# Performance work log

Hardware: AMD Instinct MI355X
Metric: run time of the kernel (lower is better)

## Reference

```python
import jax, jax.numpy as jnp
import numpy as np

N_EMBED = 384
HEAD_SIZE = 64
B, T = 128, 512


def rope(x):
    # Faithful to source: fres = 1/1000**(arange(0,dim,2)//dim) -> integer
    # floor-div makes the exponent all zeros, so fres == 1 everywhere.
    Bx, Tx, D = x.shape
    half = D // 2
    fres = jnp.ones((half,), dtype=jnp.float32)
    ang = jnp.arange(Tx, dtype=jnp.float32)[:, None] * fres[None, :]  # (T, half)
    cos, sin = jnp.cos(ang), jnp.sin(ang)
    xr = x.reshape(Bx, Tx, half, 2)
    xe, xo = xr[..., 0], xr[..., 1]
    oe = xe * cos - xo * sin
    oo = xe * sin + xo * cos
    return jnp.stack([oe, oo], axis=-1).reshape(Bx, Tx, D)


def setup_inputs() -> dict:
    key = jax.random.key(0)
    ks = jax.random.split(key, 7)
    s = 1.0 / np.sqrt(N_EMBED)
    return {
        "x": jax.random.normal(ks[0], (B, T, N_EMBED), dtype=jnp.float32),
        "wq": jax.random.uniform(ks[1], (N_EMBED, HEAD_SIZE), jnp.float32, -s, s),
        "bq": jax.random.uniform(ks[2], (HEAD_SIZE,), jnp.float32, -s, s),
        "wk": jax.random.uniform(ks[3], (N_EMBED, HEAD_SIZE), jnp.float32, -s, s),
        "bk": jax.random.uniform(ks[4], (HEAD_SIZE,), jnp.float32, -s, s),
        "wv": jax.random.uniform(ks[5], (N_EMBED, HEAD_SIZE), jnp.float32, -s, s),
        "bv": jax.random.uniform(ks[6], (HEAD_SIZE,), jnp.float32, -s, s),
    }


def reference(x, wq, bq, wk, bk, wv, bv):
    Bx, Tx, C = x.shape  # C = n_embed; scale uses C per the source (not head_size)
    q = rope(x @ wq + bq)
    k = rope(x @ wk + bk)
    wei = jnp.einsum("bqd,bkd->bqk", q, k) * (C ** -0.5)  # (B, T, T)
    causal = jnp.tril(jnp.ones((Tx, Tx), dtype=bool))
    wei = jnp.where(causal, wei, -jnp.inf)
    wei = jax.nn.softmax(wei, axis=-1)
    v = x @ wv + bv
    return jnp.einsum("bqk,bkd->bqd", wei, v)
```

## Files before the change

kernel.cpp:

```cpp
#include <hip/hip_runtime.h>

#define TSEQ 512
#define NB   128
#define CDIM 384
#define HD   64
#define QSCALE 0.051031036307982884f
#define MBIAS  8.0f

typedef _Float16 half8  __attribute__((ext_vector_type(8)));
typedef _Float16 half4  __attribute__((ext_vector_type(4)));
typedef float    floatx4 __attribute__((ext_vector_type(4)));

typedef __attribute__((address_space(3))) unsigned int lds_u32;
typedef const __attribute__((address_space(1))) unsigned int g_u32;

__device__ __forceinline__ void load_lds16(const void* g, void* l) {
    __builtin_amdgcn_global_load_lds((g_u32*)g, (lds_u32*)l, 16, 0, 0);
}

__global__ void prep_w(const float* __restrict__ wq, const float* __restrict__ wk,
                       const float* __restrict__ wv, _Float16* __restrict__ Wt)
{
    int i = blockIdx.x * 256 + threadIdx.x;
    const int per = CDIM * HD;
    if (i >= 3 * per) return;
    int mat = i / per;
    int rem = i - mat * per;
    int k = rem / HD;
    int n = rem - k * HD;
    const float* w = (mat == 0) ? wq : ((mat == 1) ? wk : wv);
    Wt[((size_t)mat * HD + n) * CDIM + k] = (_Float16)w[rem];
}

__global__ __launch_bounds__(256) void qkv_gemm(
    const float* __restrict__ x, const _Float16* __restrict__ Wt,
    const float* __restrict__ bq, const float* __restrict__ bk,
    const float* __restrict__ bv,
    _Float16* __restrict__ Qw, _Float16* __restrict__ Kw,
    _Float16* __restrict__ Vtw, int b0)
{
    __shared__ __align__(16) float    xs[8 * 64 * 8];
    __shared__ __align__(16) _Float16 wsb[8 * 192 * 8];

    const int tid  = threadIdx.x;
    const int wave = tid >> 6;
    const int lane = tid & 63;
    const int l16  = lane & 15;
    const int quad = lane >> 4;

    const int row0 = blockIdx.x * 64;
    const size_t rowg = (size_t)b0 * TSEQ + row0;

    floatx4 acc[12];
#pragma unroll
    for (int i = 0; i < 12; ++i)
#pragma unroll
        for (int r = 0; r < 4; ++r) acc[i][r] = 0.f;

    for (int c = 0; c < 6; ++c) {
        const int kk0 = c * 64;

#pragma unroll
        for (int i = 0; i < 4; ++i) {
            const int I    = wave * 4 + i;
            const int cell = I * 32 + (lane >> 1);
            const int kblk = cell >> 6;
            const int m    = cell & 63;
            const int kin0 = (lane & 1) * 4;
            const float* src = x + (rowg + m) * CDIM + kk0 + kblk * 8 + kin0;
            load_lds16(src, (char*)xs + I * 1024);
        }
#pragma unroll
        for (int i = 0; i < 6; ++i) {
            const int I2   = wave * 6 + i;
            const int c2   = I2 * 64 + lane;
            const int kblk = c2 / 192;
            const int n    = c2 - kblk * 192;
            const _Float16* src = Wt + (size_t)n * CDIM + kk0 + kblk * 8;
            load_lds16(src, (char*)wsb + I2 * 1024);
        }
        __syncthreads();

#pragma unroll
        for (int kb2 = 0; kb2 < 2; ++kb2) {
            const int kblk = kb2 * 4 + quad;
            const float* ap = xs + ((size_t)kblk * 64 + wave * 16 + l16) * 8;
            floatx4 a0 = *(const floatx4*)ap;
            floatx4 a1 = *(const floatx4*)(ap + 4);
            half8 a;
#pragma unroll
            for (int jj = 0; jj < 8; ++jj)
                a[jj] = (_Float16)(jj < 4 ? a0[jj] : a1[jj - 4]);
            const _Float16* bp = wsb + ((size_t)kblk * 192 + l16) * 8;
#pragma unroll
            for (int i = 0; i < 12; ++i) {
                half8 bb = *(const half8*)(bp + i * 128);
                acc[i] = __builtin_amdgcn_mfma_f32_16x16x32_f16(a, bb, acc[i], 0, 0, 0);
            }
        }
        __syncthreads();
    }

    float bq4[4], bk4[4], bv4[4];
#pragma unroll
    for (int s4 = 0; s4 < 4; ++s4) {
        const int cc = s4 * 16 + l16;
        bq4[s4] = bq[cc]; bk4[s4] = bk[cc]; bv4[s4] = bv[cc];
    }
    const int t00  = (row0 & (TSEQ - 1)) + wave * 16 + quad * 4;
    const int bidx = row0 >> 9;
    const int rowb = row0 + wave * 16 + quad * 4;

#pragma unroll
    for (int r = 0; r < 4; ++r) {
        const int t = t00 + r;
        const float st = sinf((float)t);
        const float ct = cosf((float)t);
        const int row = rowb + r;
#pragma unroll
        for (int s4 = 0; s4 < 4; ++s4) {
            const int cc = s4 * 16 + l16;
            float vq = acc[s4][r] + bq4[s4];
            float pq = __shfl_xor(vq, 1);
            vq = (cc & 1) ? (pq * st + vq * ct) : (vq * ct - pq * st);
            Qw[(size_t)row * HD + cc] = (_Float16)(vq * QSCALE);
            float vk = acc[4 + s4][r] + bk4[s4];
            float pk = __shfl_xor(vk, 1);
            vk = (cc & 1) ? (pk * st + vk * ct) : (vk * ct - pk * st);
            Kw[(size_t)row * HD + cc] = (_Float16)vk;
        }
    }
#pragma unroll
    for (int s4 = 0; s4 < 4; ++s4) {
        const int cc = s4 * 16 + l16;
        half4 vpack;
#pragma unroll
        for (int r = 0; r < 4; ++r) vpack[r] = (_Float16)(acc[8 + s4][r] + bv4[s4]);
        *(half4*)(Vtw + ((size_t)bidx * HD + cc) * TSEQ + t00) = vpack;
    }
}

__global__ __launch_bounds__(256) void attn_kernel(
    const _Float16* __restrict__ Qw, const _Float16* __restrict__ Kw,
    const _Float16* __restrict__ Vtw, float* __restrict__ out, int b0)
{
    const int qt   = blockIdx.x;
    const int bl   = blockIdx.y;
    const int tid  = threadIdx.x;
    const int wave = tid >> 6;
    const int lane = tid & 63;
    const int l16  = lane & 15;
    const int quad = lane >> 4;

    __shared__ __align__(16) _Float16 pbuf[4][16][72];

    const _Float16* Qb = Qw  + (size_t)bl * TSEQ * HD;
    const _Float16* Kb = Kw  + (size_t)bl * TSEQ * HD;
    const _Float16* Vb = Vtw + (size_t)bl * HD * TSEQ;

    const int qA = qt * 128 + wave * 16;
    const int qB = qA + 64;
    const int jd = 2 * qt;

    half8 aQA0 = *(const half8*)(Qb + (size_t)(qA + l16) * HD + quad * 8);
    half8 aQA1 = *(const half8*)(Qb + (size_t)(qA + l16) * HD + 32 + quad * 8);
    half8 aQB0 = *(const half8*)(Qb + (size_t)(qB + l16) * HD + quad * 8);
    half8 aQB1 = *(const half8*)(Qb + (size_t)(qB + l16) * HD + 32 + quad * 8);

    half8 ones;
#pragma unroll
    for (int jj = 0; jj < 8; ++jj) ones[jj] = (_Float16)1.f;

    floatx4 accO[8], accL[2];
#pragma unroll
    for (int i = 0; i < 8; ++i)
#pragma unroll
        for (int r = 0; r < 4; ++r) accO[i][r] = 0.f;
#pragma unroll
    for (int s = 0; s < 2; ++s)
#pragma unroll
        for (int r = 0; r < 4; ++r) accL[s][r] = 0.f;

    for (int j = 0; j <= jd + 1; ++j) {
        const int kb = j * 64;

        half8 bK0[4], bK1[4], bV0[4], bV1[4];
#pragma unroll
        for (int s4 = 0; s4 < 4; ++s4) {
            const _Float16* kp = Kb + (size_t)(kb + s4 * 16 + l16) * HD + quad * 8;
            bK0[s4] = *(const half8*)(kp);
            bK1[s4] = *(const half8*)(kp + 32);
            const _Float16* vp = Vb + (size_t)(s4 * 16 + l16) * TSEQ + kb + quad * 8;
            bV0[s4] = *(const half8*)(vp);
            bV1[s4] = *(const half8*)(vp + 32);
        }

        if (j <= jd) {
            floatx4 st4[4];
#pragma unroll
            for (int s4 = 0; s4 < 4; ++s4) {
#pragma unroll
                for (int r = 0; r < 4; ++r) st4[s4][r] = 0.f;
                st4[s4] = __builtin_amdgcn_mfma_f32_16x16x32_f16(bK0[s4], aQA0, st4[s4], 0, 0, 0);
                st4[s4] = __builtin_amdgcn_mfma_f32_16x16x32_f16(bK1[s4], aQA1, st4[s4], 0, 0, 0);
            }
            const int qrow = qA + l16;
#pragma unroll
            for (int s4 = 0; s4 < 4; ++s4) {
                half4 w;
#pragma unroll
                for (int r = 0; r < 4; ++r) {
                    float p = __expf(fminf(st4[s4][r], 18.f) - MBIAS);
                    if (j == jd) {
                        const int kcol = kb + s4 * 16 + quad * 4 + r;
                        if (kcol > qrow) p = 0.f;
                    }
                    w[r] = (_Float16)p;
                }
                *(half4*)(&pbuf[wave][l16][s4 * 16 + quad * 4]) = w;
            }
            half8 aP0 = *(const half8*)(&pbuf[wave][l16][quad * 8]);
            half8 aP1 = *(const half8*)(&pbuf[wave][l16][32 + quad * 8]);
#pragma unroll
            for (int s4 = 0; s4 < 4; ++s4) {
                accO[s4] = __builtin_amdgcn_mfma_f32_16x16x32_f16(aP0, bV0[s4], accO[s4], 0, 0, 0);
                accO[s4] = __builtin_amdgcn_mfma_f32_16x16x32_f16(aP1, bV1[s4], accO[s4], 0, 0, 0);
            }
            accL[0] = __builtin_amdgcn_mfma_f32_16x16x32_f16(aP0, ones, accL[0], 0, 0, 0);
            accL[0] = __builtin_amdgcn_mfma_f32_16x16x32_f16(aP1, ones, accL[0], 0, 0, 0);
        }

        {
            floatx4 st4[4];
#pragma unroll
            for (int s4 = 0; s4 < 4; ++s4) {
#pragma unroll
                for (int r = 0; r < 4; ++r) st4[s4][r] = 0.f;
                st4[s4] = __builtin_amdgcn_mfma_f32_16x16x32_f16(bK0[s4], aQB0, st4[s4], 0, 0, 0);
                st4[s4] = __builtin_amdgcn_mfma_f32_16x16x32_f16(bK1[s4], aQB1, st4[s4], 0, 0, 0);
            }
            const int qrow = qB + l16;
#pragma unroll
            for (int s4 = 0; s4 < 4; ++s4) {
                half4 w;
#pragma unroll
                for (int r = 0; r < 4; ++r) {
                    float p = __expf(fminf(st4[s4][r], 18.f) - MBIAS);
                    if (j == jd + 1) {
                        const int kcol = kb + s4 * 16 + quad * 4 + r;
                        if (kcol > qrow) p = 0.f;
                    }
                    w[r] = (_Float16)p;
                }
                *(half4*)(&pbuf[wave][l16][s4 * 16 + quad * 4]) = w;
            }
            half8 aP0 = *(const half8*)(&pbuf[wave][l16][quad * 8]);
            half8 aP1 = *(const half8*)(&pbuf[wave][l16][32 + quad * 8]);
#pragma unroll
            for (int s4 = 0; s4 < 4; ++s4) {
                accO[4 + s4] = __builtin_amdgcn_mfma_f32_16x16x32_f16(aP0, bV0[s4], accO[4 + s4], 0, 0, 0);
                accO[4 + s4] = __builtin_amdgcn_mfma_f32_16x16x32_f16(aP1, bV1[s4], accO[4 + s4], 0, 0, 0);
            }
            accL[1] = __builtin_amdgcn_mfma_f32_16x16x32_f16(aP0, ones, accL[1], 0, 0, 0);
            accL[1] = __builtin_amdgcn_mfma_f32_16x16x32_f16(aP1, ones, accL[1], 0, 0, 0);
        }
    }

#pragma unroll
    for (int s = 0; s < 2; ++s) {
        const int qbase = (s == 0) ? qA : qB;
        float inv[4];
#pragma unroll
        for (int r = 0; r < 4; ++r) inv[r] = 1.f / accL[s][r];
#pragma unroll
        for (int s4 = 0; s4 < 4; ++s4) {
            const int dcol = s4 * 16 + l16;
#pragma unroll
            for (int r = 0; r < 4; ++r) {
                const int qr = qbase + quad * 4 + r;
                out[((size_t)(b0 + bl) * TSEQ + qr) * HD + dcol] =
                    accO[s * 4 + s4][r] * inv[r];
            }
        }
    }
}

extern "C" void kernel_launch(void* const* d_in, const int* in_sizes, int n_in,
                              void* d_out, int out_size, void* d_ws, size_t ws_size,
                              hipStream_t stream)
{
    char* ws = (char*)d_ws;
    _Float16* Wt = (_Float16*)ws;
    char* qkv_base = ws + 147456;

    const size_t per_b = (size_t)3 * TSEQ * HD * sizeof(_Float16);
    size_t avail = (ws_size > (size_t)147456) ? ws_size - 147456 : per_b;
    int nbc = (int)(avail / per_b);
    if (nbc > NB) nbc = NB;
    if (nbc < 1)  nbc = 1;

    const size_t chunk_elems = (size_t)nbc * TSEQ * HD;
    _Float16* Qw  = (_Float16*)qkv_base;
    _Float16* Kw  = Qw + chunk_elems;
    _Float16* Vtw = Kw + chunk_elems;

    prep_w<<<dim3((3 * CDIM * HD + 255) / 256), dim3(256), 0, stream>>>(
        (const float*)d_in[1], (const float*)d_in[3], (const float*)d_in[5], Wt);

    for (int b0 = 0; b0 < NB; b0 += nbc) {
        const int nb = (NB - b0 < nbc) ? (NB - b0) : nbc;
        qkv_gemm<<<dim3(nb * 8), dim3(256), 0, stream>>>(
            (const float*)d_in[0], Wt, (const float*)d_in[2], (const float*)d_in[4],
            (const float*)d_in[6], Qw, Kw, Vtw, b0);
        attn_kernel<<<dim3(4, nb), dim3(256), 0, stream>>>(
            Qw, Kw, Vtw, (float*)d_out, b0);
    }
}
```

Measured before the change: 212.9 us.

## Split attention KV range across waves, double-buffer GEMM loads, use exp2

```diff
diff --git a/kernel.cpp b/kernel.cpp
--- a/kernel.cpp
+++ b/kernel.cpp
@@ -4,8 +4,9 @@
 #define NB   128
 #define CDIM 384
 #define HD   64
-#define QSCALE 0.051031036307982884f
-#define MBIAS  8.0f
+#define QSCALE2 0.07362222569f
+#define MBIAS2  11.541560327f
+#define SCLAMP  26.0f
 
 typedef _Float16 half8  __attribute__((ext_vector_type(8)));
 typedef _Float16 half4  __attribute__((ext_vector_type(4)));
@@ -39,8 +40,8 @@
     _Float16* __restrict__ Qw, _Float16* __restrict__ Kw,
     _Float16* __restrict__ Vtw, int b0)
 {
-    __shared__ __align__(16) float    xs[8 * 64 * 8];
-    __shared__ __align__(16) _Float16 wsb[8 * 192 * 8];
+    __shared__ __align__(16) float    xs[2][8 * 64 * 8];
+    __shared__ __align__(16) _Float16 wsb[2][8 * 192 * 8];
 
     const int tid  = threadIdx.x;
     const int wave = tid >> 6;
@@ -57,9 +58,8 @@
 #pragma unroll
         for (int r = 0; r < 4; ++r) acc[i][r] = 0.f;
 
-    for (int c = 0; c < 6; ++c) {
+    auto stage = [&](int c, int bsel) {
         const int kk0 = c * 64;
-
 #pragma unroll
         for (int i = 0; i < 4; ++i) {
             const int I    = wave * 4 + i;
@@ -68,7 +68,7 @@
             const int m    = cell & 63;
             const int kin0 = (lane & 1) * 4;
             const float* src = x + (rowg + m) * CDIM + kk0 + kblk * 8 + kin0;
-            load_lds16(src, (char*)xs + I * 1024);
+            load_lds16(src, (char*)xs + bsel * 16384 + I * 1024);
         }
 #pragma unroll
         for (int i = 0; i < 6; ++i) {
@@ -77,28 +77,32 @@
             const int kblk = c2 / 192;
             const int n    = c2 - kblk * 192;
             const _Float16* src = Wt + (size_t)n * CDIM + kk0 + kblk * 8;
-            load_lds16(src, (char*)wsb + I2 * 1024);
-        }
+            load_lds16(src, (char*)wsb + bsel * 24576 + I2 * 1024);
+        }
+    };
+
+    stage(0, 0);
+    for (int c = 0; c < 6; ++c) {
         __syncthreads();
-
+        if (c < 5) stage(c + 1, (c + 1) & 1);
+        const int bsel = c & 1;
 #pragma unroll
         for (int kb2 = 0; kb2 < 2; ++kb2) {
             const int kblk = kb2 * 4 + quad;
-            const float* ap = xs + ((size_t)kblk * 64 + wave * 16 + l16) * 8;
+            const float* ap = xs[bsel] + ((size_t)kblk * 64 + wave * 16 + l16) * 8;
             floatx4 a0 = *(const floatx4*)ap;
             floatx4 a1 = *(const floatx4*)(ap + 4);
             half8 a;
 #pragma unroll
             for (int jj = 0; jj < 8; ++jj)
                 a[jj] = (_Float16)(jj < 4 ? a0[jj] : a1[jj - 4]);
-            const _Float16* bp = wsb + ((size_t)kblk * 192 + l16) * 8;
+            const _Float16* bp = wsb[bsel] + ((size_t)kblk * 192 + l16) * 8;
 #pragma unroll
             for (int i = 0; i < 12; ++i) {
                 half8 bb = *(const half8*)(bp + i * 128);
                 acc[i] = __builtin_amdgcn_mfma_f32_16x16x32_f16(a, bb, acc[i], 0, 0, 0);
             }
         }
-        __syncthreads();
     }
 
     float bq4[4], bk4[4], bv4[4];
@@ -123,7 +127,7 @@
             float vq = acc[s4][r] + bq4[s4];
             float pq = __shfl_xor(vq, 1);
             vq = (cc & 1) ? (pq * st + vq * ct) : (vq * ct - pq * st);
-            Qw[(size_t)row * HD + cc] = (_Float16)(vq * QSCALE);
+            Qw[(size_t)row * HD + cc] = (_Float16)(vq * QSCALE2);
             float vk = acc[4 + s4][r] + bk4[s4];
             float pk = __shfl_xor(vk, 1);
             vk = (cc & 1) ? (pk * st + vk * ct) : (vk * ct - pk * st);
@@ -144,74 +148,85 @@
     const _Float16* __restrict__ Qw, const _Float16* __restrict__ Kw,
     const _Float16* __restrict__ Vtw, float* __restrict__ out, int b0)
 {
-    const int qt   = blockIdx.x;
-    const int bl   = blockIdx.y;
-    const int tid  = threadIdx.x;
-    const int wave = tid >> 6;
-    const int lane = tid & 63;
-    const int l16  = lane & 15;
-    const int quad = lane >> 4;
+    const int qtile = 7 - blockIdx.x;
+    const int bl    = blockIdx.y;
+    const int tid   = threadIdx.x;
+    const int wave  = tid >> 6;
+    const int lane  = tid & 63;
+    const int l16   = lane & 15;
+    const int quad  = lane >> 4;
 
     __shared__ __align__(16) _Float16 pbuf[4][16][72];
+    __shared__ __align__(16) float oBuf[4][64][64];
+    __shared__ float lBuf[4][64];
 
     const _Float16* Qb = Qw  + (size_t)bl * TSEQ * HD;
     const _Float16* Kb = Kw  + (size_t)bl * TSEQ * HD;
     const _Float16* Vb = Vtw + (size_t)bl * HD * TSEQ;
 
-    const int qA = qt * 128 + wave * 16;
-    const int qB = qA + 64;
-    const int jd = 2 * qt;
-
-    half8 aQA0 = *(const half8*)(Qb + (size_t)(qA + l16) * HD + quad * 8);
-    half8 aQA1 = *(const half8*)(Qb + (size_t)(qA + l16) * HD + 32 + quad * 8);
-    half8 aQB0 = *(const half8*)(Qb + (size_t)(qB + l16) * HD + quad * 8);
-    half8 aQB1 = *(const half8*)(Qb + (size_t)(qB + l16) * HD + 32 + quad * 8);
+    const int qb = qtile * 64;
+
+    half8 aQ0[4], aQ1[4];
+#pragma unroll
+    for (int st = 0; st < 4; ++st) {
+        const _Float16* qp = Qb + (size_t)(qb + st * 16 + l16) * HD + quad * 8;
+        aQ0[st] = *(const half8*)(qp);
+        aQ1[st] = *(const half8*)(qp + 32);
+    }
 
     half8 ones;
 #pragma unroll
     for (int jj = 0; jj < 8; ++jj) ones[jj] = (_Float16)1.f;
 
-    floatx4 accO[8], accL[2];
-#pragma unroll
-    for (int i = 0; i < 8; ++i)
-#pragma unroll
-        for (int r = 0; r < 4; ++r) accO[i][r] = 0.f;
-#pragma unroll
-    for (int s = 0; s < 2; ++s)
-#pragma unroll
-        for (int r = 0; r < 4; ++r) accL[s][r] = 0.f;
-
-    for (int j = 0; j <= jd + 1; ++j) {
+    floatx4 accO[4][4], accL[4];
+#pragma unroll
+    for (int st = 0; st < 4; ++st) {
+#pragma unroll
+        for (int s4 = 0; s4 < 4; ++s4)
+#pragma unroll
+            for (int r = 0; r < 4; ++r) accO[st][s4][r] = 0.f;
+#pragma unroll
+        for (int r = 0; r < 4; ++r) accL[st][r] = 0.f;
+    }
+
+    for (int j = wave; j <= qtile; j += 4) {
         const int kb = j * 64;
-
-        half8 bK0[4], bK1[4], bV0[4], bV1[4];
+        const bool diag = (j == qtile);
+
+        floatx4 st4[4][4];
 #pragma unroll
         for (int s4 = 0; s4 < 4; ++s4) {
             const _Float16* kp = Kb + (size_t)(kb + s4 * 16 + l16) * HD + quad * 8;
-            bK0[s4] = *(const half8*)(kp);
-            bK1[s4] = *(const half8*)(kp + 32);
+            half8 bK0 = *(const half8*)(kp);
+            half8 bK1 = *(const half8*)(kp + 32);
+#pragma unroll
+            for (int st = 0; st < 4; ++st) {
+                floatx4 z;
+#pragma unroll
+                for (int r = 0; r < 4; ++r) z[r] = 0.f;
+                z = __builtin_amdgcn_mfma_f32_16x16x32_f16(bK0, aQ0[st], z, 0, 0, 0);
+                st4[st][s4] = __builtin_amdgcn_mfma_f32_16x16x32_f16(bK1, aQ1[st], z, 0, 0, 0);
+            }
+        }
+
+        half8 bV0[4], bV1[4];
+#pragma unroll
+        for (int s4 = 0; s4 < 4; ++s4) {
             const _Float16* vp = Vb + (size_t)(s4 * 16 + l16) * TSEQ + kb + quad * 8;
             bV0[s4] = *(const half8*)(vp);
             bV1[s4] = *(const half8*)(vp + 32);
         }
 
-        if (j <= jd) {
-            floatx4 st4[4];
-#pragma unroll
-            for (int s4 = 0; s4 < 4; ++s4) {
-#pragma unroll
-                for (int r = 0; r < 4; ++r) st4[s4][r] = 0.f;
-                st4[s4] = __builtin_amdgcn_mfma_f32_16x16x32_f16(bK0[s4], aQA0, st4[s4], 0, 0, 0);
-                st4[s4] = __builtin_amdgcn_mfma_f32_16x16x32_f16(bK1[s4], aQA1, st4[s4], 0, 0, 0);
-            }
-            const int qrow = qA + l16;
+#pragma unroll
+        for (int st = 0; st < 4; ++st) {
+            const int qrow = qb + st * 16 + l16;
 #pragma unroll
             for (int s4 = 0; s4 < 4; ++s4) {
                 half4 w;
 #pragma unroll
                 for (int r = 0; r < 4; ++r) {
-                    float p = __expf(fminf(st4[s4][r], 18.f) - MBIAS);
-                    if (j == jd) {
+                    float p = exp2f(fminf(st4[st][s4][r], SCLAMP) - MBIAS2);
+                    if (diag) {
                         const int kcol = kb + s4 * 16 + quad * 4 + r;
                         if (kcol > qrow) p = 0.f;
                     }
@@ -223,65 +238,38 @@
             half8 aP1 = *(const half8*)(&pbuf[wave][l16][32 + quad * 8]);
 #pragma unroll
             for (int s4 = 0; s4 < 4; ++s4) {
-                accO[s4] = __builtin_amdgcn_mfma_f32_16x16x32_f16(aP0, bV0[s4], accO[s4], 0, 0, 0);
-                accO[s4] = __builtin_amdgcn_mfma_f32_16x16x32_f16(aP1, bV1[s4], accO[s4], 0, 0, 0);
+                accO[st][s4] = __builtin_amdgcn_mfma_f32_16x16x32_f16(aP0, bV0[s4], accO[st][s4], 0, 0, 0);
+                accO[st][s4] = __builtin_amdgcn_mfma_f32_16x16x32_f16(aP1, bV1[s4], accO[st][s4], 0, 0, 0);
             }
-            accL[0] = __builtin_amdgcn_mfma_f32_16x16x32_f16(aP0, ones, accL[0], 0, 0, 0);
-            accL[0] = __builtin_amdgcn_mfma_f32_16x16x32_f16(aP1, ones, accL[0], 0, 0, 0);
-        }
-
-        {
-            floatx4 st4[4];
-#pragma unroll
-            for (int s4 = 0; s4 < 4; ++s4) {
-#pragma unroll
-                for (int r = 0; r < 4; ++r) st4[s4][r] = 0.f;
-                st4[s4] = __builtin_amdgcn_mfma_f32_16x16x32_f16(bK0[s4], aQB0, st4[s4], 0, 0, 0);
-                st4[s4] = __builtin_amdgcn_mfma_f32_16x16x32_f16(bK1[s4], aQB1, st4[s4], 0, 0, 0);
-            }
-            const int qrow = qB + l16;
-#pragma unroll
-            for (int s4 = 0; s4 < 4; ++s4) {
-                half4 w;
-#pragma unroll
-                for (int r = 0; r < 4; ++r) {
-                    float p = __expf(fminf(st4[s4][r], 18.f) - MBIAS);
-                    if (j == jd + 1) {
-                        const int kcol = kb + s4 * 16 + quad * 4 + r;
-                        if (kcol > qrow) p = 0.f;
-                    }
-                    w[r] = (_Float16)p;
-                }
-                *(half4*)(&pbuf[wave][l16][s4 * 16 + quad * 4]) = w;
-            }
-            half8 aP0 = *(const half8*)(&pbuf[wave][l16][quad * 8]);
-            half8 aP1 = *(const half8*)(&pbuf[wave][l16][32 + quad * 8]);
-#pragma unroll
-            for (int s4 = 0; s4 < 4; ++s4) {
-                accO[4 + s4] = __builtin_amdgcn_mfma_f32_16x16x32_f16(aP0, bV0[s4], accO[4 + s4], 0, 0, 0);
-                accO[4 + s4] = __builtin_amdgcn_mfma_f32_16x16x32_f16(aP1, bV1[s4], accO[4 + s4], 0, 0, 0);
-            }
-            accL[1] = __builtin_amdgcn_mfma_f32_16x16x32_f16(aP0, ones, accL[1], 0, 0, 0);
-            accL[1] = __builtin_amdgcn_mfma_f32_16x16x32_f16(aP1, ones, accL[1], 0, 0, 0);
-        }
-    }
-
-#pragma unroll
-    for (int s = 0; s < 2; ++s) {
-        const int qbase = (s == 0) ? qA : qB;
-        float inv[4];
-#pragma unroll
-        for (int r = 0; r < 4; ++r) inv[r] = 1.f / accL[s][r];
-#pragma unroll
-        for (int s4 = 0; s4 < 4; ++s4) {
-            const int dcol = s4 * 16 + l16;
-#pragma unroll
-            for (int r = 0; r < 4; ++r) {
-                const int qr = qbase + quad * 4 + r;
-                out[((size_t)(b0 + bl) * TSEQ + qr) * HD + dcol] =
-                    accO[s * 4 + s4][r] * inv[r];
-            }
-        }
+            accL[st] = __builtin_amdgcn_mfma_f32_16x16x32_f16(aP0, ones, accL[st], 0, 0, 0);
+            accL[st] = __builtin_amdgcn_mfma_f32_16x16x32_f16(aP1, ones, accL[st], 0, 0, 0);
+        }
+    }
+
+#pragma unroll
+    for (int st = 0; st < 4; ++st) {
+#pragma unroll
+        for (int s4 = 0; s4 < 4; ++s4)
+#pragma unroll
+            for (int r = 0; r < 4; ++r)
+                oBuf[wave][st * 16 + quad * 4 + r][s4 * 16 + l16] = accO[st][s4][r];
+        if (l16 == 0)
+#pragma unroll
+            for (int r = 0; r < 4; ++r)
+                lBuf[wave][st * 16 + quad * 4 + r] = accL[st][r];
+    }
+    __syncthreads();
+
+    const size_t obase = ((size_t)(b0 + bl) * TSEQ + qb) * HD;
+#pragma unroll
+    for (int it = 0; it < 16; ++it) {
+        const int e   = it * 256 + tid;
+        const int row = e >> 6;
+        const int col = e & 63;
+        const float o = oBuf[0][row][col] + oBuf[1][row][col] +
+                        oBuf[2][row][col] + oBuf[3][row][col];
+        const float l = lBuf[0][row] + lBuf[1][row] + lBuf[2][row] + lBuf[3][row];
+        out[obase + (size_t)row * HD + col] = o / l;
     }
 }
 
@@ -312,7 +300,7 @@
         qkv_gemm<<<dim3(nb * 8), dim3(256), 0, stream>>>(
             (const float*)d_in[0], Wt, (const float*)d_in[2], (const float*)d_in[4],
             (const float*)d_in[6], Qw, Kw, Vtw, b0);
-        attn_kernel<<<dim3(4, nb), dim3(256), 0, stream>>>(
+        attn_kernel<<<dim3(8, nb), dim3(256), 0, stream>>>(
             Qw, Kw, Vtw, (float*)d_out, b0);
     }
 }
```

After: 231.9 us. 1.09x slower.
